# Kernel optimization log

Measured on AMD Instinct MI355X. Metric: run time of the kernel, lower is better.

The kernel has to match this reference:

```python
import jax, jax.numpy as jnp
import numpy as np

MARGIN = 0.5
N_CLASSES = 100

def setup_inputs() -> dict:
    key = jax.random.key(0)
    k1, k2 = jax.random.split(key)
    n, d = 8192, 128
    inputs = jax.random.normal(k1, (n, d), dtype=jnp.float32)
    targets = jax.random.randint(k2, (n,), 0, N_CLASSES, dtype=jnp.int64)
    return {"inputs": inputs, "targets": targets}

def reference(inputs, targets):
    # pairwise squared euclidean distances: [n, n]
    sq = jnp.sum(inputs * inputs, axis=1)  # [n]
    dist = sq[:, None] + sq[None, :] - 2.0 * (inputs @ inputs.T)
    dist = jnp.maximum(dist, 0.0)
    # positive mask: same label (diagonal included, matching original)
    mask = targets[:, None] == targets[None, :]  # [n, n] bool
    big = jnp.float32(1e30)
    dist_ap = jnp.max(jnp.where(mask, dist, -big), axis=1)  # hardest positive per row
    dist_an = jnp.min(jnp.where(mask, big, dist), axis=1)   # hardest negative per row
    loss = jnp.sum(jax.nn.relu(dist_ap - dist_an + MARGIN))
    return loss
```

## Files before the change

### kernel.cpp

```cpp
#include <hip/hip_runtime.h>
#include <hip/hip_bf16.h>

#define D 128
#define MARGIN 0.5f
#define NSPLIT 16
#define JSPAN 512

typedef __attribute__((ext_vector_type(8))) short bf16x8;
typedef __attribute__((ext_vector_type(4))) float f32x4;

__global__ void prep_kernel(const float* __restrict__ x,
                            float* __restrict__ sq,
                            __hip_bfloat16* __restrict__ xb,
                            float* __restrict__ out, int n) {
    int tid = threadIdx.x;
    int row = blockIdx.x * 4 + (tid >> 6);
    int lane = tid & 63;
    const float2* xr = (const float2*)(x + (size_t)row * D);
    float2 v = xr[lane];
    __hip_bfloat162 b2;
    b2.x = __float2bfloat16(v.x);
    b2.y = __float2bfloat16(v.y);
    ((__hip_bfloat162*)(xb + (size_t)row * D))[lane] = b2;
    float s = v.x * v.x + v.y * v.y;
    #pragma unroll
    for (int o = 32; o > 0; o >>= 1) s += __shfl_xor(s, o, 64);
    if (lane == 0) sq[row] = s;
    if (blockIdx.x == 0 && tid == 0) *out = 0.0f;
}

__launch_bounds__(256, 4)
__global__ void gram_kernel(const __hip_bfloat16* __restrict__ xb,
                            const float* __restrict__ sq,
                            const int* __restrict__ tgt,
                            float* __restrict__ pap,
                            float* __restrict__ pan, int n) {
    __shared__ __align__(16) __hip_bfloat16 Bs[4][32 * D];
    __shared__ float sqs[JSPAN];
    __shared__ int   tgs[JSPAN];

    const int tid  = threadIdx.x;
    const int wid  = tid >> 6;
    const int lane = tid & 63;
    const int quad = lane >> 4;
    const int l    = lane & 15;
    const int i0   = blockIdx.x * 128;
    const int j0   = blockIdx.y * JSPAN;
    const int rowbase = i0 + wid * 32;

    bf16x8 afrag[2][4];
    {
        const __hip_bfloat16* abase = xb + (size_t)(rowbase + l) * D + quad * 8;
        #pragma unroll
        for (int mt = 0; mt < 2; ++mt)
            #pragma unroll
            for (int ks = 0; ks < 4; ++ks)
                afrag[mt][ks] = *(const bf16x8*)(abase + (size_t)mt * 16 * D + ks * 32);
    }

    int li[2][4];
    #pragma unroll
    for (int mt = 0; mt < 2; ++mt)
        #pragma unroll
        for (int reg = 0; reg < 4; ++reg)
            li[mt][reg] = tgt[rowbase + mt * 16 + quad * 4 + reg];

    float lap[8], lan[8];
    #pragma unroll
    for (int k = 0; k < 8; ++k) { lap[k] = -1e30f; lan[k] = 1e30f; }

    const char* xbb = (const char*)xb;

    #define PREF_HALF(h)                                                      \
        do {                                                                  \
            const int s_ = (h) & 3;                                           \
            _Pragma("unroll")                                                 \
            for (int i_ = 0; i_ < 2; ++i_) {                                  \
                int q_ = wid * 128 + i_ * 64 + lane;                          \
                int r_ = q_ >> 4;                                             \
                int c_ = (q_ & 15) ^ (r_ & 15);                               \
                const char* g_ = xbb + (size_t)(j0 + (h) * 32 + r_) * 256     \
                                     + (size_t)c_ * 16;                       \
                char* l_ = (char*)Bs + (size_t)s_ * 8192                      \
                         + (size_t)(wid * 128 + i_ * 64) * 16;                \
                __builtin_amdgcn_global_load_lds(                             \
                    (const __attribute__((address_space(1))) void*)g_,        \
                    (__attribute__((address_space(3))) void*)l_, 16, 0, 0);   \
            }                                                                 \
        } while (0)

    #define COMP_HALF(h)                                                      \
        do {                                                                  \
            const char* Bb_ = (const char*)Bs + (size_t)((h) & 3) * 8192;     \
            _Pragma("unroll")                                                 \
            for (int jt = 0; jt < 2; ++jt) {                                  \
                f32x4 acc0 = (f32x4){0.f, 0.f, 0.f, 0.f};                     \
                f32x4 acc1 = (f32x4){0.f, 0.f, 0.f, 0.f};                     \
                __builtin_amdgcn_s_setprio(1);                                \
                _Pragma("unroll")                                             \
                for (int ks = 0; ks < 4; ++ks) {                              \
                    int q = (jt * 16 + l) * 16 + ((ks * 4 + quad) ^ l);       \
                    bf16x8 bfr = *(const bf16x8*)(Bb_ + (size_t)q * 16);      \
                    acc0 = __builtin_amdgcn_mfma_f32_16x16x32_bf16(           \
                        afrag[0][ks], bfr, acc0, 0, 0, 0);                    \
                    acc1 = __builtin_amdgcn_mfma_f32_16x16x32_bf16(           \
                        afrag[1][ks], bfr, acc1, 0, 0, 0);                    \
                }                                                             \
                __builtin_amdgcn_s_setprio(0);                                \
                int jb_ = (h) * 32 + jt * 16;                                 \
                float sjc = sqs[jb_ + l];                                     \
                int   tjc = tgs[jb_ + l];                                     \
                _Pragma("unroll")                                             \
                for (int reg = 0; reg < 4; ++reg) {                           \
                    float t0 = fmaf(-2.0f, acc0[reg], sjc);                   \
                    float t1 = fmaf(-2.0f, acc1[reg], sjc);                   \
                    bool s0 = (li[0][reg] == tjc);                            \
                    bool s1 = (li[1][reg] == tjc);                            \
                    lap[reg]     = fmaxf(lap[reg],     s0 ? t0 : -1e30f);     \
                    lan[reg]     = fminf(lan[reg],     s0 ? 1e30f : t0);      \
                    lap[4 + reg] = fmaxf(lap[4 + reg], s1 ? t1 : -1e30f);     \
                    lan[4 + reg] = fminf(lan[4 + reg], s1 ? 1e30f : t1);      \
                }                                                             \
            }                                                                 \
        } while (0)

    PREF_HALF(0);
    PREF_HALF(1);
    PREF_HALF(2);
    sqs[tid]       = sq[j0 + tid];
    sqs[tid + 256] = sq[j0 + tid + 256];
    tgs[tid]       = tgt[j0 + tid];
    tgs[tid + 256] = tgt[j0 + tid + 256];

    {
        int rnd = ((blockIdx.y * gridDim.x + blockIdx.x) >> 8) & 3;
        #pragma unroll 1
        for (int i = 0; i < rnd; ++i) __builtin_amdgcn_s_sleep(15);
    }
    asm volatile("s_waitcnt lgkmcnt(0)" ::: "memory");

    for (int h = 0; h < 14; ++h) {
        asm volatile("s_waitcnt vmcnt(4)" ::: "memory");
        __builtin_amdgcn_s_barrier();
        asm volatile("" ::: "memory");
        if (h < 13) PREF_HALF(h + 3);
        COMP_HALF(h);
    }
    asm volatile("s_waitcnt vmcnt(2)" ::: "memory");
    __builtin_amdgcn_s_barrier();
    asm volatile("" ::: "memory");
    COMP_HALF(14);
    asm volatile("s_waitcnt vmcnt(0)" ::: "memory");
    __builtin_amdgcn_s_barrier();
    asm volatile("" ::: "memory");
    COMP_HALF(15);

    #undef PREF_HALF
    #undef COMP_HALF

    #pragma unroll
    for (int mt = 0; mt < 2; ++mt)
        #pragma unroll
        for (int reg = 0; reg < 4; ++reg) {
            float p = lap[mt * 4 + reg], q = lan[mt * 4 + reg];
            #pragma unroll
            for (int o = 1; o < 16; o <<= 1) {
                p = fmaxf(p, __shfl_xor(p, o, 64));
                q = fminf(q, __shfl_xor(q, o, 64));
            }
            if (l == mt * 4 + reg) {
                int gi = rowbase + mt * 16 + quad * 4 + reg;
                float s = sq[gi];
                pap[(size_t)blockIdx.y * n + gi] = fmaxf(s + p, 0.0f);
                pan[(size_t)blockIdx.y * n + gi] = fmaxf(s + q, 0.0f);
            }
        }
}

__global__ void final_kernel(const float* __restrict__ pap,
                             const float* __restrict__ pan,
                             float* __restrict__ out, int n) {
    int i = blockIdx.x * blockDim.x + threadIdx.x;
    float p = pap[i], q = pan[i];
    #pragma unroll
    for (int s = 1; s < NSPLIT; ++s) {
        p = fmaxf(p, pap[(size_t)s * n + i]);
        q = fminf(q, pan[(size_t)s * n + i]);
    }
    float v = fmaxf(p - q + MARGIN, 0.0f);
    #pragma unroll
    for (int o = 32; o > 0; o >>= 1) v += __shfl_xor(v, o, 64);
    __shared__ float ws[4];
    int lane = threadIdx.x & 63, w = threadIdx.x >> 6;
    if (lane == 0) ws[w] = v;
    __syncthreads();
    if (threadIdx.x == 0) atomicAdd(out, ws[0] + ws[1] + ws[2] + ws[3]);
}

extern "C" void kernel_launch(void* const* d_in, const int* in_sizes, int n_in,
                              void* d_out, int out_size, void* d_ws, size_t ws_size,
                              hipStream_t stream) {
    const float* x   = (const float*)d_in[0];
    const int*   tgt = (const int*)d_in[1];
    float* out = (float*)d_out;
    const int n = in_sizes[1];

    float*          sq  = (float*)d_ws;
    float*          pap = (float*)((char*)d_ws + (size_t)n * 4);
    float*          pan = (float*)((char*)d_ws + (size_t)n * 4 + (size_t)n * NSPLIT * 4);
    __hip_bfloat16* xb  = (__hip_bfloat16*)((char*)d_ws + (size_t)n * 4 + (size_t)n * NSPLIT * 8);

    prep_kernel<<<n / 4, 256, 0, stream>>>(x, sq, xb, out, n);
    dim3 grid(n / 128, NSPLIT);
    gram_kernel<<<grid, 256, 0, stream>>>(xb, sq, tgt, pap, pan, n);
    final_kernel<<<n / 256, 256, 0, stream>>>(pap, pan, out, n);
}
```

Measured before the change: 87.49 us.

## Exploit Gram symmetry by computing only upper-triangle tiles with dual row/column reductions

New measurement: 161.1 us. 84.2% more time.

```diff
diff --git a/kernel.cpp b/kernel.cpp
--- a/kernel.cpp
+++ b/kernel.cpp
@@ -3,8 +3,9 @@
 
 #define D 128
 #define MARGIN 0.5f
-#define NSPLIT 16
-#define JSPAN 512
+#define JW 256
+#define NWIN 32
+#define NBI 64
 
 typedef __attribute__((ext_vector_type(8))) short bf16x8;
 typedef __attribute__((ext_vector_type(4))) float f32x4;
@@ -12,6 +13,8 @@
 __global__ void prep_kernel(const float* __restrict__ x,
                             float* __restrict__ sq,
                             __hip_bfloat16* __restrict__ xb,
+                            float* __restrict__ pap, float* __restrict__ pan,
+                            float* __restrict__ pap2, float* __restrict__ pan2,
                             float* __restrict__ out, int n) {
     int tid = threadIdx.x;
     int row = blockIdx.x * 4 + (tid >> 6);
@@ -26,6 +29,11 @@
     #pragma unroll
     for (int o = 32; o > 0; o >>= 1) s += __shfl_xor(s, o, 64);
     if (lane == 0) sq[row] = s;
+
+    int g = blockIdx.x * 256 + tid;
+    pap2[g] = 0.0f;
+    pan2[g] = 1e30f;
+    if (g < n * NWIN) { pap[g] = 0.0f; pan[g] = 1e30f; }
     if (blockIdx.x == 0 && tid == 0) *out = 0.0f;
 }
 
@@ -34,18 +42,25 @@
                             const float* __restrict__ sq,
                             const int* __restrict__ tgt,
                             float* __restrict__ pap,
-                            float* __restrict__ pan, int n) {
+                            float* __restrict__ pan,
+                            float* __restrict__ pap2,
+                            float* __restrict__ pan2, int n) {
     __shared__ __align__(16) __hip_bfloat16 Bs[4][32 * D];
-    __shared__ float sqs[JSPAN];
-    __shared__ int   tgs[JSPAN];
+    __shared__ float sqs[JW];
+    __shared__ int   tgs[JW];
 
     const int tid  = threadIdx.x;
     const int wid  = tid >> 6;
     const int lane = tid & 63;
     const int quad = lane >> 4;
     const int l    = lane & 15;
-    const int i0   = blockIdx.x * 128;
-    const int j0   = blockIdx.y * JSPAN;
+
+    int bi = 0, rem = blockIdx.x;
+    while (rem >= NWIN - (bi >> 1)) { rem -= NWIN - (bi >> 1); ++bi; }
+    const int by = (bi >> 1) + rem;
+
+    const int i0 = bi * 128;
+    const int j0 = by * JW;
     const int rowbase = i0 + wid * 32;
 
     bf16x8 afrag[2][4];
@@ -59,15 +74,22 @@
     }
 
     int li[2][4];
+    float siv[2][4];
     #pragma unroll
     for (int mt = 0; mt < 2; ++mt)
         #pragma unroll
-        for (int reg = 0; reg < 4; ++reg)
-            li[mt][reg] = tgt[rowbase + mt * 16 + quad * 4 + reg];
+        for (int reg = 0; reg < 4; ++reg) {
+            int r = rowbase + mt * 16 + quad * 4 + reg;
+            li[mt][reg]  = tgt[r];
+            siv[mt][reg] = sq[r];
+        }
 
     float lap[8], lan[8];
     #pragma unroll
     for (int k = 0; k < 8; ++k) { lap[k] = -1e30f; lan[k] = 1e30f; }
+    float jpreg[4], jnreg[4];
+    #pragma unroll
+    for (int k = 0; k < 4; ++k) { jpreg[k] = -1e30f; jnreg[k] = 1e30f; }
 
     const char* xbb = (const char*)xb;
 
@@ -107,19 +129,39 @@
                         afrag[1][ks], bfr, acc1, 0, 0, 0);                    \
                 }                                                             \
                 __builtin_amdgcn_s_setprio(0);                                \
-                int jb_ = (h) * 32 + jt * 16;                                 \
+                const int jb_ = (h) * 32 + jt * 16;                           \
                 float sjc = sqs[jb_ + l];                                     \
                 int   tjc = tgs[jb_ + l];                                     \
+                float jp = -1e30f, jn = 1e30f;                                \
                 _Pragma("unroll")                                             \
                 for (int reg = 0; reg < 4; ++reg) {                           \
-                    float t0 = fmaf(-2.0f, acc0[reg], sjc);                   \
-                    float t1 = fmaf(-2.0f, acc1[reg], sjc);                   \
+                    float a0 = acc0[reg], a1 = acc1[reg];                     \
+                    float t0 = fmaf(-2.0f, a0, sjc);                          \
+                    float t1 = fmaf(-2.0f, a1, sjc);                          \
+                    float u0 = fmaf(-2.0f, a0, siv[0][reg]);                  \
+                    float u1 = fmaf(-2.0f, a1, siv[1][reg]);                  \
                     bool s0 = (li[0][reg] == tjc);                            \
                     bool s1 = (li[1][reg] == tjc);                            \
                     lap[reg]     = fmaxf(lap[reg],     s0 ? t0 : -1e30f);     \
                     lan[reg]     = fminf(lan[reg],     s0 ? 1e30f : t0);      \
                     lap[4 + reg] = fmaxf(lap[4 + reg], s1 ? t1 : -1e30f);     \
                     lan[4 + reg] = fminf(lan[4 + reg], s1 ? 1e30f : t1);      \
+                    jp = fmaxf(jp, s0 ? u0 : -1e30f);                         \
+                    jp = fmaxf(jp, s1 ? u1 : -1e30f);                         \
+                    jn = fminf(jn, s0 ? 1e30f : u0);                          \
+                    jn = fminf(jn, s1 ? 1e30f : u1);                          \
+                }                                                             \
+                jp = fmaxf(jp, __shfl_xor(jp, 16, 64));                       \
+                jp = fmaxf(jp, __shfl_xor(jp, 32, 64));                       \
+                jn = fminf(jn, __shfl_xor(jn, 16, 64));                       \
+                jn = fminf(jn, __shfl_xor(jn, 32, 64));                       \
+                {                                                             \
+                    const int cw = (((h) * 2 + jt) & 3);                      \
+                    const int rw = (((h) * 2 + jt) >> 2);                     \
+                    jpreg[rw] = (quad == cw) ? fmaxf(jpreg[rw], jp)           \
+                                             : jpreg[rw];                     \
+                    jnreg[rw] = (quad == cw) ? fminf(jnreg[rw], jn)           \
+                                             : jnreg[rw];                     \
                 }                                                             \
             }                                                                 \
         } while (0)
@@ -127,33 +169,26 @@
     PREF_HALF(0);
     PREF_HALF(1);
     PREF_HALF(2);
-    sqs[tid]       = sq[j0 + tid];
-    sqs[tid + 256] = sq[j0 + tid + 256];
-    tgs[tid]       = tgt[j0 + tid];
-    tgs[tid + 256] = tgt[j0 + tid + 256];
-
-    {
-        int rnd = ((blockIdx.y * gridDim.x + blockIdx.x) >> 8) & 3;
-        #pragma unroll 1
-        for (int i = 0; i < rnd; ++i) __builtin_amdgcn_s_sleep(15);
-    }
+    sqs[tid] = sq[j0 + tid];
+    tgs[tid] = tgt[j0 + tid];
     asm volatile("s_waitcnt lgkmcnt(0)" ::: "memory");
 
-    for (int h = 0; h < 14; ++h) {
+    #pragma unroll
+    for (int h = 0; h < 6; ++h) {
         asm volatile("s_waitcnt vmcnt(4)" ::: "memory");
         __builtin_amdgcn_s_barrier();
         asm volatile("" ::: "memory");
-        if (h < 13) PREF_HALF(h + 3);
+        if (h < 5) PREF_HALF(h + 3);
         COMP_HALF(h);
     }
     asm volatile("s_waitcnt vmcnt(2)" ::: "memory");
     __builtin_amdgcn_s_barrier();
     asm volatile("" ::: "memory");
-    COMP_HALF(14);
+    COMP_HALF(6);
     asm volatile("s_waitcnt vmcnt(0)" ::: "memory");
     __builtin_amdgcn_s_barrier();
     asm volatile("" ::: "memory");
-    COMP_HALF(15);
+    COMP_HALF(7);
 
     #undef PREF_HALF
     #undef COMP_HALF
@@ -170,22 +205,49 @@
             }
             if (l == mt * 4 + reg) {
                 int gi = rowbase + mt * 16 + quad * 4 + reg;
-                float s = sq[gi];
-                pap[(size_t)blockIdx.y * n + gi] = fmaxf(s + p, 0.0f);
-                pan[(size_t)blockIdx.y * n + gi] = fmaxf(s + q, 0.0f);
+                float s = siv[mt][reg];
+                pap[(size_t)by * n + gi] = fmaxf(s + p, 0.0f);
+                pan[(size_t)by * n + gi] = fmaxf(s + q, 0.0f);
             }
         }
+
+    __syncthreads();
+    float* scr = (float*)Bs;
+    #pragma unroll
+    for (int r = 0; r < 4; ++r) {
+        int w = (r * 4 + quad) * 16 + l;
+        scr[wid * 256 + w]        = jpreg[r];
+        scr[1024 + wid * 256 + w] = jnreg[r];
+    }
+    __syncthreads();
+    {
+        int w = tid;
+        float p2 = fmaxf(fmaxf(scr[w], scr[256 + w]),
+                         fmaxf(scr[512 + w], scr[768 + w]));
+        float n2 = fminf(fminf(scr[1024 + w], scr[1280 + w]),
+                         fminf(scr[1536 + w], scr[1792 + w]));
+        float sj = sqs[w];
+        pap2[(size_t)bi * n + j0 + w] = fmaxf(sj + p2, 0.0f);
+        pan2[(size_t)bi * n + j0 + w] = fmaxf(sj + n2, 0.0f);
+    }
 }
 
 __global__ void final_kernel(const float* __restrict__ pap,
                              const float* __restrict__ pan,
+                             const float* __restrict__ pap2,
+                             const float* __restrict__ pan2,
                              float* __restrict__ out, int n) {
     int i = blockIdx.x * blockDim.x + threadIdx.x;
     float p = pap[i], q = pan[i];
-    #pragma unroll
-    for (int s = 1; s < NSPLIT; ++s) {
+    #pragma unroll 4
+    for (int s = 1; s < NWIN; ++s) {
         p = fmaxf(p, pap[(size_t)s * n + i]);
         q = fminf(q, pan[(size_t)s * n + i]);
+    }
+    #pragma unroll 4
+    for (int b = 0; b < NBI; ++b) {
+        p = fmaxf(p, pap2[(size_t)b * n + i]);
+        q = fminf(q, pan2[(size_t)b * n + i]);
     }
     float v = fmaxf(p - q + MARGIN, 0.0f);
     #pragma unroll
@@ -205,13 +267,17 @@
     float* out = (float*)d_out;
     const int n = in_sizes[1];
 
-    float*          sq  = (float*)d_ws;
-    float*          pap = (float*)((char*)d_ws + (size_t)n * 4);
-    float*          pan = (float*)((char*)d_ws + (size_t)n * 4 + (size_t)n * NSPLIT * 4);
-    __hip_bfloat16* xb  = (__hip_bfloat16*)((char*)d_ws + (size_t)n * 4 + (size_t)n * NSPLIT * 8);
-
-    prep_kernel<<<n / 4, 256, 0, stream>>>(x, sq, xb, out, n);
-    dim3 grid(n / 128, NSPLIT);
-    gram_kernel<<<grid, 256, 0, stream>>>(xb, sq, tgt, pap, pan, n);
-    final_kernel<<<n / 256, 256, 0, stream>>>(pap, pan, out, n);
-}
+    float* sq   = (float*)d_ws;
+    float* pap  = sq + n;
+    float* pan  = pap + (size_t)NWIN * n;
+    float* pap2 = pan + (size_t)NWIN * n;
+    float* pan2 = pap2 + (size_t)NBI * n;
+    __hip_bfloat16* xb = (__hip_bfloat16*)(pan2 + (size_t)NBI * n);
+
+    int nblk = 0;
+    for (int b = 0; b < NBI; ++b) nblk += NWIN - (b >> 1);
+
+    prep_kernel<<<n / 4, 256, 0, stream>>>(x, sq, xb, pap, pan, pap2, pan2, out, n);
+    gram_kernel<<<nblk, 256, 0, stream>>>(xb, sq, tgt, pap, pan, pap2, pan2, n);
+    final_kernel<<<n / 256, 256, 0, stream>>>(pap, pan, pap2, pan2, out, n);
+}
```
